# Optimization experiments

Hardware: AMD Instinct MI355X
Metric: run time of the kernel (lower is better)

Reference implementation:

```python
import jax, jax.numpy as jnp
import numpy as np

B, H, W, C = 2, 128, 128, 128
NS = 8                      # attn_num_splits
WH, WW = H // NS, W // NS   # window size 16x16
SH, SW = WH // 2, WW // 2   # shift sizes
HID = 2 * C * 4             # ffn hidden (in_channels = 2*d_model, expansion 4)
EPS = 1e-5


def _make_swin_mask():
    # Standard shifted-window attention mask: -100 between different regions.
    img = np.zeros((H, W), np.int32)
    cnt = 0
    for hs in (slice(0, -WH), slice(-WH, -SH), slice(-SH, None)):
        for ws in (slice(0, -WW), slice(-WW, -SW), slice(-SW, None)):
            img[hs, ws] = cnt
            cnt += 1
    ids = img.reshape(NS, WH, NS, WW).transpose(0, 2, 1, 3).reshape(NS * NS, WH * WW)
    mask = np.where(ids[:, None, :] != ids[:, :, None], -100.0, 0.0).astype(np.float32)
    return jnp.asarray(mask)  # (64, 256, 256)


def _layernorm(x, g, b):
    m = jnp.mean(x, axis=-1, keepdims=True)
    v = jnp.mean(jnp.square(x - m), axis=-1, keepdims=True)
    return (x - m) * jax.lax.rsqrt(v + EPS) * g + b


def setup_inputs() -> dict:
    key = jax.random.key(0)
    ks = jax.random.split(key, 8)
    s = 1.0 / np.sqrt(C)
    return {
        "source": jax.random.normal(ks[0], (B, H * W, C), jnp.float32),
        "target": jax.random.normal(ks[1], (B, H * W, C), jnp.float32),
        "Wq": jax.random.normal(ks[2], (C, C), jnp.float32) * s,
        "Wk": jax.random.normal(ks[3], (C, C), jnp.float32) * s,
        "Wv": jax.random.normal(ks[4], (C, C), jnp.float32) * s,
        "Wm": jax.random.normal(ks[5], (C, C), jnp.float32) * s,
        "g1": jnp.ones((C,), jnp.float32),
        "b1": jnp.zeros((C,), jnp.float32),
        "W1": jax.random.normal(ks[6], (2 * C, HID), jnp.float32) * (1.0 / np.sqrt(2 * C)),
        "W2": jax.random.normal(ks[7], (HID, C), jnp.float32) * (1.0 / np.sqrt(HID)),
        "g2": jnp.ones((C,), jnp.float32),
        "b2": jnp.zeros((C,), jnp.float32),
        "shifted_window_attn_mask": _make_swin_mask(),
        "height": H,
        "width": W,
        "attn_num_splits": NS,
    }


def reference(source, target, Wq, Wk, Wv, Wm, g1, b1, W1, W2, g2, b2,
              shifted_window_attn_mask, height, width, attn_num_splits):
    b, L, c = source.shape
    h, w, ns = height, width, attn_num_splits
    wh, ww = h // ns, w // ns
    sh, sw = wh // 2, ww // 2

    q = source @ Wq
    k = target @ Wk
    v = target @ Wv

    def to_windows(x):
        # (b, h*w, c) -> shifted -> (b, nWin, wh*ww, c)
        x = x.reshape(b, h, w, c)
        x = jnp.roll(x, (-sh, -sw), axis=(1, 2))
        x = x.reshape(b, ns, wh, ns, ww, c).transpose(0, 1, 3, 2, 4, 5)
        return x.reshape(b, ns * ns, wh * ww, c)

    qw, kw, vw = to_windows(q), to_windows(k), to_windows(v)
    scores = jnp.einsum('bnlc,bnmc->bnlm', qw, kw) / (c ** 0.5)
    scores = scores + shifted_window_attn_mask[None]  # broadcast over batch
    attn = jax.nn.softmax(scores, axis=-1)
    out = jnp.einsum('bnlm,bnmc->bnlc', attn, vw)

    # merge windows back and undo the shift
    out = out.reshape(b, ns, ns, wh, ww, c).transpose(0, 1, 3, 2, 4, 5).reshape(b, h, w, c)
    out = jnp.roll(out, (sh, sw), axis=(1, 2)).reshape(b, h * w, c)

    message = _layernorm(out @ Wm, g1, b1)
    ffn_in = jnp.concatenate([source, message], axis=-1)
    message = jax.nn.gelu(ffn_in @ W1, approximate=False) @ W2
    message = _layernorm(message, g2, b2)
    return source + message
```

## Files before the change

kernel.cpp:

```cpp
#include <hip/hip_runtime.h>
#include <math.h>
#include <stdint.h>


typedef unsigned short u16;
typedef __attribute__((ext_vector_type(8))) short bf16x8;
typedef __attribute__((ext_vector_type(4))) float f32x4;
typedef __attribute__((ext_vector_type(4))) short u16x4;
typedef __attribute__((ext_vector_type(2))) unsigned int u32x2;

__device__ __forceinline__ u16 f2b(float f) {
    unsigned int i = __float_as_uint(f);
    unsigned int r = (i + 0x7fffu + ((i >> 16) & 1u)) >> 16;
    return (u16)r;
}

__device__ __forceinline__ bf16x8 pk8(f32x4 a, f32x4 b) {
    union { bf16x8 v; unsigned u[4]; } r;
    asm("v_cvt_pk_bf16_f32 %0, %1, %2" : "=v"(r.u[0]) : "v"(a[0]), "v"(a[1]));
    asm("v_cvt_pk_bf16_f32 %0, %1, %2" : "=v"(r.u[1]) : "v"(a[2]), "v"(a[3]));
    asm("v_cvt_pk_bf16_f32 %0, %1, %2" : "=v"(r.u[2]) : "v"(b[0]), "v"(b[1]));
    asm("v_cvt_pk_bf16_f32 %0, %1, %2" : "=v"(r.u[3]) : "v"(b[2]), "v"(b[3]));
    return r.v;
}

__device__ __forceinline__ float gelu_e(float x) {
    float y = fabsf(x) * 0.70710678118f;
    float u = fmaf(y, fmaf(y, fmaf(y, fmaf(y, 0.078108f, 0.000972f),
                                   0.230389f), 0.278393f), 1.0f);
    u = u * u; u = u * u;
    float r = __builtin_amdgcn_rcpf(u);
    return fmaxf(x, 0.f) - 0.5f * fabsf(x) * r;
}

__device__ __forceinline__ void cp16(const void* g, void* l) {
    auto* gp = reinterpret_cast<const __attribute__((address_space(1))) unsigned int*>(
        reinterpret_cast<uintptr_t>(g));
    auto* lp = reinterpret_cast<__attribute__((address_space(3))) unsigned int*>(
        reinterpret_cast<uintptr_t>(l));
    __builtin_amdgcn_global_load_lds(gp, lp, 16, 0, 0);
}

__device__ __forceinline__ int win_map(int gm) {
    int b = gm >> 14, rr = gm & 16383;
    int win = rr >> 8, t = rr & 255;
    int wi = win >> 3, wj = win & 7, i = t >> 4, j = t & 15;
    int h = (wi * 16 + i + 8) & 127;
    int w = (wj * 16 + j + 8) & 127;
    return (b << 14) + h * 128 + w;
}

__global__ __launch_bounds__(256, 3)
void gemm_qkv(const float* __restrict__ srcf, const float* __restrict__ tgtf,
              const u16* __restrict__ Bt, u16* __restrict__ qw,
              u16* __restrict__ kw, u16* __restrict__ vwt)
{
    __shared__ __align__(16) u16 SMEM[17408];
    u16* Bs = SMEM;
    u16* Ts = SMEM;

    const int tid = threadIdx.x;
    const int w = tid >> 6, lane = tid & 63;
    const int lm = lane & 15, q = lane >> 4;
    const int wm = w >> 1, wn = w & 1;
    const int m0 = blockIdx.x * 128;
    const int y = blockIdx.y;
    const float* Af = (y == 0) ? srcf : tgtf;

#pragma unroll
    for (int s = 0; s < 4; ++s)
#pragma unroll
        for (int i = 0; i < 2; ++i) {
            int row = w * 32 + i * 16 + (lane >> 2);
            int kc = s * 32 + (lane & 3) * 8;
            cp16(Bt + (size_t)(y * 128 + row) * 128 + kc,
                 (void*)(Bs + (s * 128 + w * 32 + i * 16) * 32));
        }

    bf16x8 af[4][4];
#pragma unroll
    for (int t = 0; t < 4; ++t) {
        const float* ap = Af + (size_t)win_map(m0 + wm * 64 + t * 16 + lm) * 128;
#pragma unroll
        for (int s = 0; s < 4; ++s) {
            f32x4 a = *(const f32x4*)(ap + s * 32 + q * 8);
            f32x4 b = *(const f32x4*)(ap + s * 32 + q * 8 + 4);
            af[t][s] = pk8(a, b);
        }
    }
    __syncthreads();

    f32x4 acc[4][4] = {};
    __builtin_amdgcn_s_setprio(1);
#pragma unroll
    for (int s = 0; s < 4; ++s) {
        bf16x8 bfr[4];
#pragma unroll
        for (int t = 0; t < 4; ++t)
            bfr[t] = *(const bf16x8*)(Bs + (s * 128 + wn * 64 + t * 16 + lm) * 32 + q * 8);
#pragma unroll
        for (int mt = 0; mt < 4; ++mt)
#pragma unroll
            for (int nt = 0; nt < 4; ++nt)
                acc[mt][nt] = __builtin_amdgcn_mfma_f32_16x16x32_bf16(
                    af[mt][s], bfr[nt], acc[mt][nt], 0, 0, 0);
    }
    __builtin_amdgcn_s_setprio(0);

    __syncthreads();
#pragma unroll
    for (int mt = 0; mt < 4; ++mt)
#pragma unroll
        for (int nt = 0; nt < 4; ++nt)
#pragma unroll
            for (int r = 0; r < 4; ++r) {
                int rowl = wm * 64 + mt * 16 + q * 4 + r;
                int col = wn * 64 + nt * 16 + lm;
                int idx = (y == 2) ? col * 136 + rowl : rowl * 136 + col;
                Ts[idx] = f2b(acc[mt][nt][r]);
            }
    __syncthreads();
    const int c8 = (tid & 15) * 8;
#pragma unroll
    for (int i = 0; i < 8; ++i) {
        int rr = i * 16 + (tid >> 4);
        bf16x8 t = *(const bf16x8*)(Ts + rr * 136 + c8);
        if (y == 2) {
            int wix = m0 >> 8, tok0 = m0 & 255;
            *(bf16x8*)(vwt + (size_t)wix * 32768 + (size_t)rr * 256 + tok0 + c8) = t;
        } else {
            u16* Cv = (y == 0) ? qw : kw;
            *(bf16x8*)(Cv + (size_t)(m0 + rr) * 128 + c8) = t;
        }
    }
}

__global__ __launch_bounds__(256, 2)
void attn_msg(const u16* __restrict__ qw, const u16* __restrict__ kw,
              const u16* __restrict__ vt, const u16* __restrict__ wmt,
              const float* __restrict__ g, const float* __restrict__ bb,
              u16* __restrict__ msgb)
{
    __shared__ __align__(16) u16 Ps[64 * 264];
    __shared__ __align__(16) u16 B32[16384];

    const int tid = threadIdx.x, w = tid >> 6, lane = tid & 63;
    const int lm = lane & 15, q = lane >> 4;
    const int l4r = lane >> 2, l4c = (lane & 3) * 8;
    const int bid = blockIdx.x;
    const int qc = bid >> 7;
    const int gwin = bid & 127;
    const int win = gwin & 63, b = gwin >> 6;
    const int wi = win >> 3, wj = win & 7;
    const int q0 = qc * 64;
    const size_t wbase = (size_t)(b * 64 + win);
    const u16* kwb = kw + wbase * 256 * 128;
    const u16* qwb = qw + wbase * 256 * 128;
    const u16* vtb = vt + wbase * 128 * 256;

    u16* Qs = Ps;
#pragma unroll
    for (int i = 0; i < 4; ++i)
        cp16(qwb + (size_t)(q0 + w * 16 + l4r) * 128 + i * 32 + l4c,
             (void*)(Qs + (i * 64 + w * 16) * 32));
#pragma unroll
    for (int s = 0; s < 4; ++s)
#pragma unroll
        for (int i = 0; i < 2; ++i) {
            int tok = w * 32 + i * 16 + l4r;
            cp16(kwb + (size_t)tok * 128 + s * 32 + l4c,
                 (void*)(B32 + (s * 128 + w * 32 + i * 16) * 32));
        }
    __syncthreads();

    bf16x8 af[4];
#pragma unroll
    for (int kt = 0; kt < 4; ++kt)
        af[kt] = *(const bf16x8*)(Qs + (kt * 64 + w * 16 + lm) * 32 + q * 8);
    __syncthreads();

#pragma unroll
    for (int ss = 0; ss < 4; ++ss)
#pragma unroll
        for (int i = 0; i < 2; ++i) {
            int tok = 128 + w * 32 + i * 16 + l4r;
            cp16(kwb + (size_t)tok * 128 + ss * 32 + l4c,
                 (void*)(Ps + (ss * 128 + w * 32 + i * 16) * 32));
        }

    f32x4 s[16];
#pragma unroll
    for (int nt = 0; nt < 16; ++nt) { f32x4 z = {0.f, 0.f, 0.f, 0.f}; s[nt] = z; }
    __builtin_amdgcn_s_setprio(1);
#pragma unroll
    for (int kt = 0; kt < 4; ++kt)
#pragma unroll
        for (int nt = 0; nt < 8; ++nt) {
            bf16x8 bf = *(const bf16x8*)(B32 + (kt * 128 + nt * 16 + lm) * 32 + q * 8);
            s[nt] = __builtin_amdgcn_mfma_f32_16x16x32_bf16(af[kt], bf, s[nt], 0, 0, 0);
        }
    __builtin_amdgcn_s_setprio(0);
    __syncthreads();

#pragma unroll
    for (int tt = 0; tt < 4; ++tt)
#pragma unroll
        for (int i = 0; i < 2; ++i) {
            int ch = w * 32 + i * 16 + l4r;
            cp16(vtb + (size_t)ch * 256 + tt * 32 + l4c,
                 (void*)(B32 + (tt * 128 + w * 32 + i * 16) * 32));
        }
    __builtin_amdgcn_s_setprio(1);
#pragma unroll
    for (int kt = 0; kt < 4; ++kt)
#pragma unroll
        for (int nt = 8; nt < 16; ++nt) {
            bf16x8 bf = *(const bf16x8*)(Ps + (kt * 128 + (nt - 8) * 16 + lm) * 32 + q * 8);
            s[nt] = __builtin_amdgcn_mfma_f32_16x16x32_bf16(af[kt], bf, s[nt], 0, 0, 0);
        }
    __builtin_amdgcn_s_setprio(0);
    __syncthreads();

    int idk[16];
#pragma unroll
    for (int nt = 0; nt < 16; ++nt) {
        int rh = (wi == 7) ? ((nt >= 8) ? 2 : 1) : 0;
        int rw = (wj == 7) ? ((lm >= 8) ? 2 : 1) : 0;
        idk[nt] = rh * 3 + rw;
    }
    const float scale = 0.08838834764831845f;
#pragma unroll
    for (int r = 0; r < 4; ++r) {
        int tq = q0 + w * 16 + q * 4 + r;
        int iq = tq >> 4, jq = tq & 15;
        int rhq = (wi == 7) ? ((iq >= 8) ? 2 : 1) : 0;
        int rwq = (wj == 7) ? ((jq >= 8) ? 2 : 1) : 0;
        int idq = rhq * 3 + rwq;
        float sv[16];
        float mx = -1e30f;
#pragma unroll
        for (int nt = 0; nt < 16; ++nt) {
            float x = s[nt][r] * scale + ((idq != idk[nt]) ? -100.f : 0.f);
            sv[nt] = x; mx = fmaxf(mx, x);
        }
        mx = fmaxf(mx, __shfl_xor(mx, 1));
        mx = fmaxf(mx, __shfl_xor(mx, 2));
        mx = fmaxf(mx, __shfl_xor(mx, 4));
        mx = fmaxf(mx, __shfl_xor(mx, 8));
        float sum = 0.f;
#pragma unroll
        for (int nt = 0; nt < 16; ++nt) { float e = __expf(sv[nt] - mx); sv[nt] = e; sum += e; }
        sum += __shfl_xor(sum, 1);
        sum += __shfl_xor(sum, 2);
        sum += __shfl_xor(sum, 4);
        sum += __shfl_xor(sum, 8);
        float inv = 1.0f / sum;
#pragma unroll
        for (int nt = 0; nt < 16; ++nt)
            Ps[(w * 16 + q * 4 + r) * 264 + nt * 16 + lm] = f2b(sv[nt] * inv);
    }

    f32x4 o[8];
#pragma unroll
    for (int nt = 0; nt < 8; ++nt) { f32x4 z = {0.f, 0.f, 0.f, 0.f}; o[nt] = z; }
    __builtin_amdgcn_s_setprio(1);
#pragma unroll
    for (int tt = 0; tt < 4; ++tt) {
        bf16x8 pf = *(const bf16x8*)(Ps + (w * 16 + lm) * 264 + tt * 32 + q * 8);
#pragma unroll
        for (int nt = 0; nt < 8; ++nt) {
            bf16x8 vf = *(const bf16x8*)(B32 + (tt * 128 + nt * 16 + lm) * 32 + q * 8);
            o[nt] = __builtin_amdgcn_mfma_f32_16x16x32_bf16(pf, vf, o[nt], 0, 0, 0);
        }
    }
    __builtin_amdgcn_s_setprio(0);
    __syncthreads();
#pragma unroll
    for (int tt = 0; tt < 4; ++tt)
#pragma unroll
        for (int i = 0; i < 2; ++i) {
            int ch = w * 32 + i * 16 + l4r;
            cp16(vtb + (size_t)ch * 256 + 128 + tt * 32 + l4c,
                 (void*)(B32 + (tt * 128 + w * 32 + i * 16) * 32));
        }
    __syncthreads();
    __builtin_amdgcn_s_setprio(1);
#pragma unroll
    for (int tt = 4; tt < 8; ++tt) {
        bf16x8 pf = *(const bf16x8*)(Ps + (w * 16 + lm) * 264 + tt * 32 + q * 8);
#pragma unroll
        for (int nt = 0; nt < 8; ++nt) {
            bf16x8 vf = *(const bf16x8*)(B32 + ((tt - 4) * 128 + nt * 16 + lm) * 32 + q * 8);
            o[nt] = __builtin_amdgcn_mfma_f32_16x16x32_bf16(pf, vf, o[nt], 0, 0, 0);
        }
    }
    __builtin_amdgcn_s_setprio(0);
    __syncthreads();

#pragma unroll
    for (int ss = 0; ss < 4; ++ss)
#pragma unroll
        for (int i = 0; i < 2; ++i) {
            int n = w * 32 + i * 16 + l4r;
            cp16(wmt + (size_t)n * 128 + ss * 32 + l4c,
                 (void*)(B32 + (ss * 128 + w * 32 + i * 16) * 32));
        }
    u16* Ot = Ps;
#pragma unroll
    for (int r = 0; r < 4; ++r) {
        int rl = w * 16 + q * 4 + r;
#pragma unroll
        for (int nt = 0; nt < 8; ++nt)
            Ot[rl * 136 + nt * 16 + lm] = f2b(o[nt][r]);
    }
    __syncthreads();

    f32x4 macc[8];
#pragma unroll
    for (int n2 = 0; n2 < 8; ++n2) { f32x4 z = {0.f, 0.f, 0.f, 0.f}; macc[n2] = z; }
    __builtin_amdgcn_s_setprio(1);
#pragma unroll
    for (int kt = 0; kt < 4; ++kt) {
        bf16x8 paf = *(const bf16x8*)(Ot + (w * 16 + lm) * 136 + kt * 32 + q * 8);
#pragma unroll
        for (int n2 = 0; n2 < 8; ++n2) {
            bf16x8 wf = *(const bf16x8*)(B32 + (kt * 128 + n2 * 16 + lm) * 32 + q * 8);
            macc[n2] = __builtin_amdgcn_mfma_f32_16x16x32_bf16(paf, wf, macc[n2], 0, 0, 0);
        }
    }
    __builtin_amdgcn_s_setprio(0);

    float gv[8], bv[8];
#pragma unroll
    for (int n2 = 0; n2 < 8; ++n2) {
        int col = n2 * 16 + lm;
        gv[n2] = g[col]; bv[n2] = bb[col];
    }
#pragma unroll
    for (int r = 0; r < 4; ++r) {
        float s1 = 0.f, s2 = 0.f;
#pragma unroll
        for (int n2 = 0; n2 < 8; ++n2) {
            float v = macc[n2][r];
            s1 += v; s2 += v * v;
        }
        s1 += __shfl_xor(s1, 1); s2 += __shfl_xor(s2, 1);
        s1 += __shfl_xor(s1, 2); s2 += __shfl_xor(s2, 2);
        s1 += __shfl_xor(s1, 4); s2 += __shfl_xor(s2, 4);
        s1 += __shfl_xor(s1, 8); s2 += __shfl_xor(s2, 8);
        float mean = s1 * (1.f / 128.f);
        float var = fmaxf(s2 * (1.f / 128.f) - mean * mean, 0.f);
        float rs = rsqrtf(var + 1e-5f);
        int t = q0 + w * 16 + q * 4 + r;
        int ii = t >> 4, jj = t & 15;
        int h = (wi * 16 + ii + 8) & 127;
        int w2 = (wj * 16 + jj + 8) & 127;
        size_t orow = ((size_t)b * 16384 + h * 128 + w2) * 128;
#pragma unroll
        for (int n2 = 0; n2 < 8; ++n2)
            msgb[orow + n2 * 16 + lm] = f2b((macc[n2][r] - mean) * rs * gv[n2] + bv[n2]);
    }
}

__global__ __launch_bounds__(512, 4)
void fused_ffn(const float* __restrict__ A0f, const u16* __restrict__ A1,
               const u16* __restrict__ W1T, const u16* __restrict__ W2T,
               const float* __restrict__ g, const float* __restrict__ bb,
               const float* __restrict__ resid, float* __restrict__ outv)
{
    __shared__ __align__(16) u16 W1s[16384];
    __shared__ __align__(16) u16 W2s[16384];
    __shared__ __align__(16) u16 Gs[4096];

    const int tid = threadIdx.x;
    const int w = tid >> 6, lane = tid & 63;
    const int lm = lane & 15, q = lane >> 4;
    const int l4r = lane >> 2, l4c = (lane & 3) * 8;
    const int wm = w >> 2, wn = w & 3;
    const int m0 = blockIdx.x * 64;

    const u16* w1p = W1T + (size_t)l4r * 256 + w * 32 + l4c;
    const u16* w2p = W2T + (size_t)((w & 3) * 32 + l4r) * 1024 + (w >> 2) * 32 + l4c;
    u16* const w1d = W1s + (w * 64) * 32;
    u16* const w2d0 = W2s + (((w >> 2) * 128 + (w & 3) * 32)) * 32;
    u16* const w2d1 = w2d0 + 8192;

    bf16x8 areg[2][8];
#pragma unroll
    for (int mt = 0; mt < 2; ++mt) {
        const int row = m0 + wm * 32 + mt * 16 + lm;
        const float* ap = A0f + (size_t)row * 128;
#pragma unroll
        for (int ks = 0; ks < 4; ++ks) {
            f32x4 a = *(const f32x4*)(ap + ks * 32 + q * 8);
            f32x4 b = *(const f32x4*)(ap + ks * 32 + q * 8 + 4);
            areg[mt][ks] = pk8(a, b);
        }
#pragma unroll
        for (int ks = 4; ks < 8; ++ks)
            areg[mt][ks] = *(const bf16x8*)(
                A1 + (size_t)row * 128 + (ks & 3) * 32 + q * 8);
    }

#pragma unroll
    for (int i = 0; i < 4; ++i)
        cp16(w1p + (size_t)(i * 16) * 256, w1d + (i * 16) * 32);
#pragma unroll
    for (int i = 0; i < 2; ++i)
        cp16(w2p + (size_t)(i * 16) * 1024, w2d0 + (i * 16) * 32);
    w1p += 16384; w2p += 64;
    __syncthreads();

    f32x4 acc2[2][2] = {};
#pragma unroll 2
    for (int c = 0; c < 16; ++c) {
        const int cb = c & 1, nb = cb ^ 1;

        {
            f32x4 acc1[2] = {};
            __builtin_amdgcn_s_setprio(1);
#pragma unroll
            for (int ks = 0; ks < 8; ++ks) {
                bf16x8 w1f = *(const bf16x8*)(W1s + (ks * 64 + wn * 16 + lm) * 32 + q * 8);
#pragma unroll
                for (int mt = 0; mt < 2; ++mt)
                    acc1[mt] = __builtin_amdgcn_mfma_f32_16x16x32_bf16(
                        w1f, areg[mt][ks], acc1[mt], 0, 0, 0);
            }
            __builtin_amdgcn_s_setprio(0);
#pragma unroll
            for (int mt = 0; mt < 2; ++mt) {
                float g0 = gelu_e(acc1[mt][0]), g1 = gelu_e(acc1[mt][1]);
                float g2 = gelu_e(acc1[mt][2]), g3 = gelu_e(acc1[mt][3]);
                unsigned p0, p1;
                asm("v_cvt_pk_bf16_f32 %0, %1, %2" : "=v"(p0) : "v"(g0), "v"(g1));
                asm("v_cvt_pk_bf16_f32 %0, %1, %2" : "=v"(p1) : "v"(g2), "v"(g3));
                int tok = wm * 32 + mt * 16 + lm;
                int slot = (wn * 2 + (q >> 1)) ^ (tok & 7);
                u32x2 pk; pk[0] = p0; pk[1] = p1;
                *(u32x2*)(Gs + tok * 64 + slot * 8 + (q & 1) * 4) = pk;
            }
        }
        __syncthreads();

        if (c + 1 < 16) {
#pragma unroll
            for (int i = 0; i < 4; ++i)
                cp16(w1p + (size_t)(i * 16) * 256, w1d + (i * 16) * 32);
            u16* d = nb ? w2d1 : w2d0;
#pragma unroll
            for (int i = 0; i < 2; ++i)
                cp16(w2p + (size_t)(i * 16) * 1024, d + (i * 16) * 32);
        }
        w1p += 16384; w2p += 64;

        {
            const u16* W2c = W2s + cb * 8192;
            __builtin_amdgcn_s_setprio(1);
#pragma unroll
            for (int ks = 0; ks < 2; ++ks) {
                bf16x8 pa[2], wf[2];
#pragma unroll
                for (int mt = 0; mt < 2; ++mt) {
                    int tok = wm * 32 + mt * 16 + lm;
                    pa[mt] = *(const bf16x8*)(Gs + tok * 64 + (((ks * 4 + q) ^ (tok & 7)) * 8));
                }
#pragma unroll
                for (int nt = 0; nt < 2; ++nt)
                    wf[nt] = *(const bf16x8*)(W2c + (ks * 128 + wn * 32 + nt * 16 + lm) * 32 + q * 8);
#pragma unroll
                for (int mt = 0; mt < 2; ++mt)
#pragma unroll
                    for (int nt = 0; nt < 2; ++nt)
                        acc2[mt][nt] = __builtin_amdgcn_mfma_f32_16x16x32_bf16(
                            pa[mt], wf[nt], acc2[mt][nt], 0, 0, 0);
            }
            __builtin_amdgcn_s_setprio(0);
        }
        __syncthreads();
    }

    float* stats = (float*)Gs;
#pragma unroll
    for (int mt = 0; mt < 2; ++mt)
#pragma unroll
        for (int r = 0; r < 4; ++r) {
            float s1 = 0.f, s2 = 0.f;
#pragma unroll
            for (int nt = 0; nt < 2; ++nt) {
                float v = acc2[mt][nt][r];
                s1 += v; s2 += v * v;
            }
            s1 += __shfl_xor(s1, 1); s2 += __shfl_xor(s2, 1);
            s1 += __shfl_xor(s1, 2); s2 += __shfl_xor(s2, 2);
            s1 += __shfl_xor(s1, 4); s2 += __shfl_xor(s2, 4);
            s1 += __shfl_xor(s1, 8); s2 += __shfl_xor(s2, 8);
            if (lm == 0) {
                int row = wm * 32 + mt * 16 + q * 4 + r;
                stats[row * 8 + wn * 2] = s1;
                stats[row * 8 + wn * 2 + 1] = s2;
            }
        }
    __syncthreads();

    float gv[2], bv[2];
#pragma unroll
    for (int nt = 0; nt < 2; ++nt) {
        int col = wn * 32 + nt * 16 + lm;
        gv[nt] = g[col]; bv[nt] = bb[col];
    }
#pragma unroll
    for (int mt = 0; mt < 2; ++mt)
#pragma unroll
        for (int r = 0; r < 4; ++r) {
            int row = wm * 32 + mt * 16 + q * 4 + r;
            f32x4 st0 = *(const f32x4*)(stats + row * 8);
            f32x4 st1 = *(const f32x4*)(stats + row * 8 + 4);
            float s1 = st0[0] + st0[2] + st1[0] + st1[2];
            float s2 = st0[1] + st0[3] + st1[1] + st1[3];
            float mean = s1 * (1.f / 128.f);
            float var = fmaxf(s2 * (1.f / 128.f) - mean * mean, 0.f);
            float rs = rsqrtf(var + 1e-5f);
#pragma unroll
            for (int nt = 0; nt < 2; ++nt) {
                int col = wn * 32 + nt * 16 + lm;
                size_t gi = (size_t)(m0 + row) * 128 + col;
                outv[gi] = (acc2[mt][nt][r] - mean) * rs * gv[nt] + bv[nt] + resid[gi];
            }
        }
}

__global__ void prep_all(const float* __restrict__ Wq, const float* __restrict__ Wk,
                         const float* __restrict__ Wv, const float* __restrict__ Wm,
                         const float* __restrict__ W1, const float* __restrict__ W2,
                         u16* __restrict__ ws)
{
    __shared__ float T[64][65];
    int bx = blockIdx.x;
    const int t = threadIdx.x;
    const float* sp; u16* dst; int R, C, r0, c0;
    if (bx < 16) {
        int m = bx >> 2, tt = bx & 3;
        sp = (m == 0) ? Wq : (m == 1) ? Wk : (m == 2) ? Wv : Wm;
        R = 128; C = 128; r0 = (tt >> 1) * 64; c0 = (tt & 1) * 64;
        dst = ws + m * 16384;
    } else if (bx < 80) {
        int tt = bx - 16;
        sp = W1; R = 256; C = 1024;
        r0 = (tt >> 4) * 64; c0 = (tt & 15) * 64;
        dst = ws + 65536;
    } else {
        int tt = bx - 80;
        sp = W2; R = 1024; C = 128;
        r0 = (tt >> 1) * 64; c0 = (tt & 1) * 64;
        dst = ws + 327680;
    }
#pragma unroll
    for (int i = 0; i < 16; ++i) {
        int idx = i * 256 + t, r = idx >> 6, c = idx & 63;
        T[r][c] = sp[(size_t)(r0 + r) * C + c0 + c];
    }
    __syncthreads();
#pragma unroll
    for (int i = 0; i < 16; ++i) {
        int idx = i * 256 + t, n = idx >> 6, k = idx & 63;
        dst[(size_t)(c0 + n) * R + r0 + k] = f2b(T[k][n]);
    }
}

#define OFF_WQT  0u
#define OFF_WMT  49152u
#define OFF_W1T  65536u
#define OFF_W2T  327680u
#define OFF_QW   458752u
#define OFF_KW   4653056u
#define OFF_VWT  8847360u
#define OFF_MSGB 13041664u

extern "C" void kernel_launch(void* const* d_in, const int* in_sizes, int n_in,
                              void* d_out, int out_size, void* d_ws, size_t ws_size,
                              hipStream_t stream)
{
    (void)in_sizes; (void)n_in; (void)out_size; (void)ws_size;
    const float* source = (const float*)d_in[0];
    const float* target = (const float*)d_in[1];
    const float* Wq = (const float*)d_in[2];
    const float* Wk = (const float*)d_in[3];
    const float* Wv = (const float*)d_in[4];
    const float* Wm = (const float*)d_in[5];
    const float* g1 = (const float*)d_in[6];
    const float* b1 = (const float*)d_in[7];
    const float* W1 = (const float*)d_in[8];
    const float* W2 = (const float*)d_in[9];
    const float* g2 = (const float*)d_in[10];
    const float* b2 = (const float*)d_in[11];
    u16* ws = (u16*)d_ws;
    float* out = (float*)d_out;

    prep_all<<<112, 256, 0, stream>>>(Wq, Wk, Wv, Wm, W1, W2, ws);
    gemm_qkv<<<dim3(256, 3), 256, 0, stream>>>(
        source, target, ws + OFF_WQT,
        ws + OFF_QW, ws + OFF_KW, ws + OFF_VWT);
    attn_msg<<<512, 256, 0, stream>>>(
        ws + OFF_QW, ws + OFF_KW, ws + OFF_VWT, ws + OFF_WMT, g1, b1,
        ws + OFF_MSGB);
    fused_ffn<<<512, 512, 0, stream>>>(
        source, ws + OFF_MSGB, ws + OFF_W1T, ws + OFF_W2T,
        g2, b2, source, out);
}
```

Baseline: 187.3 us.

## Share target tile for K and V projections, pre-convert source to bf16

The QKV projection now runs with two grid rows instead of three. The block that loads the target tile computes both K and V from the same bf16 registers, so target is read and converted only once. The source activation is converted to bf16 once in the prep kernel and then reused by both the Q projection and the FFN, which halves their activation read bytes but adds an extra conversion pass and a workspace buffer. attn_msg also loads Q directly from global into registers and issues both K halves' async copies together, removing one shared-memory round trip and a barrier.

```diff
diff --git a/kernel.cpp b/kernel.cpp
--- a/kernel.cpp
+++ b/kernel.cpp
@@ -51,7 +51,7 @@
 }
 
 __global__ __launch_bounds__(256, 3)
-void gemm_qkv(const float* __restrict__ srcf, const float* __restrict__ tgtf,
+void gemm_qkv(const u16* __restrict__ srcb, const float* __restrict__ tgtf,
               const u16* __restrict__ Bt, u16* __restrict__ qw,
               u16* __restrict__ kw, u16* __restrict__ vwt)
 {
@@ -65,7 +65,7 @@
     const int wm = w >> 1, wn = w & 1;
     const int m0 = blockIdx.x * 128;
     const int y = blockIdx.y;
-    const float* Af = (y == 0) ? srcf : tgtf;
+    const int c8 = (tid & 15) * 8;
 
 #pragma unroll
     for (int s = 0; s < 4; ++s)
@@ -78,14 +78,24 @@
         }
 
     bf16x8 af[4][4];
-#pragma unroll
-    for (int t = 0; t < 4; ++t) {
-        const float* ap = Af + (size_t)win_map(m0 + wm * 64 + t * 16 + lm) * 128;
-#pragma unroll
-        for (int s = 0; s < 4; ++s) {
-            f32x4 a = *(const f32x4*)(ap + s * 32 + q * 8);
-            f32x4 b = *(const f32x4*)(ap + s * 32 + q * 8 + 4);
-            af[t][s] = pk8(a, b);
+    if (y == 0) {
+#pragma unroll
+        for (int t = 0; t < 4; ++t) {
+            const u16* ap = srcb + (size_t)win_map(m0 + wm * 64 + t * 16 + lm) * 128;
+#pragma unroll
+            for (int s = 0; s < 4; ++s)
+                af[t][s] = *(const bf16x8*)(ap + s * 32 + q * 8);
+        }
+    } else {
+#pragma unroll
+        for (int t = 0; t < 4; ++t) {
+            const float* ap = tgtf + (size_t)win_map(m0 + wm * 64 + t * 16 + lm) * 128;
+#pragma unroll
+            for (int s = 0; s < 4; ++s) {
+                f32x4 a = *(const f32x4*)(ap + s * 32 + q * 8);
+                f32x4 b = *(const f32x4*)(ap + s * 32 + q * 8 + 4);
+                af[t][s] = pk8(a, b);
+            }
         }
     }
     __syncthreads();
@@ -106,8 +116,8 @@
                     af[mt][s], bfr[nt], acc[mt][nt], 0, 0, 0);
     }
     __builtin_amdgcn_s_setprio(0);
-
-    __syncthreads();
+    __syncthreads();
+
 #pragma unroll
     for (int mt = 0; mt < 4; ++mt)
 #pragma unroll
@@ -116,21 +126,69 @@
             for (int r = 0; r < 4; ++r) {
                 int rowl = wm * 64 + mt * 16 + q * 4 + r;
                 int col = wn * 64 + nt * 16 + lm;
-                int idx = (y == 2) ? col * 136 + rowl : rowl * 136 + col;
-                Ts[idx] = f2b(acc[mt][nt][r]);
-            }
-    __syncthreads();
-    const int c8 = (tid & 15) * 8;
-#pragma unroll
-    for (int i = 0; i < 8; ++i) {
-        int rr = i * 16 + (tid >> 4);
-        bf16x8 t = *(const bf16x8*)(Ts + rr * 136 + c8);
-        if (y == 2) {
+                Ts[rowl * 136 + col] = f2b(acc[mt][nt][r]);
+            }
+    __syncthreads();
+    {
+        u16* Cv = (y == 0) ? qw : kw;
+#pragma unroll
+        for (int i = 0; i < 8; ++i) {
+            int rr = i * 16 + (tid >> 4);
+            bf16x8 t = *(const bf16x8*)(Ts + rr * 136 + c8);
+            *(bf16x8*)(Cv + (size_t)(m0 + rr) * 128 + c8) = t;
+        }
+    }
+
+    if (y == 1) {
+        __syncthreads();
+#pragma unroll
+        for (int s = 0; s < 4; ++s)
+#pragma unroll
+            for (int i = 0; i < 2; ++i) {
+                int row = w * 32 + i * 16 + (lane >> 2);
+                int kc = s * 32 + (lane & 3) * 8;
+                cp16(Bt + (size_t)(256 + row) * 128 + kc,
+                     (void*)(Bs + (s * 128 + w * 32 + i * 16) * 32));
+            }
+        __syncthreads();
+
+        f32x4 acc2[4][4] = {};
+        __builtin_amdgcn_s_setprio(1);
+#pragma unroll
+        for (int s = 0; s < 4; ++s) {
+            bf16x8 bfr[4];
+#pragma unroll
+            for (int t = 0; t < 4; ++t)
+                bfr[t] = *(const bf16x8*)(Bs + (s * 128 + wn * 64 + t * 16 + lm) * 32 + q * 8);
+#pragma unroll
+            for (int mt = 0; mt < 4; ++mt)
+#pragma unroll
+                for (int nt = 0; nt < 4; ++nt)
+                    acc2[mt][nt] = __builtin_amdgcn_mfma_f32_16x16x32_bf16(
+                        af[mt][s], bfr[nt], acc2[mt][nt], 0, 0, 0);
+        }
+        __builtin_amdgcn_s_setprio(0);
+        __syncthreads();
+
+#pragma unroll
+        for (int mt = 0; mt < 4; ++mt)
+#pragma unroll
+            for (int nt = 0; nt < 4; ++nt)
+#pragma unroll
+                for (int r = 0; r < 4; ++r) {
+                    int rowl = wm * 64 + mt * 16 + q * 4 + r;
+                    int col = wn * 64 + nt * 16 + lm;
+                    Ts[col * 136 + rowl] = f2b(acc2[mt][nt][r]);
+                }
+        __syncthreads();
+        {
             int wix = m0 >> 8, tok0 = m0 & 255;
-            *(bf16x8*)(vwt + (size_t)wix * 32768 + (size_t)rr * 256 + tok0 + c8) = t;
-        } else {
-            u16* Cv = (y == 0) ? qw : kw;
-            *(bf16x8*)(Cv + (size_t)(m0 + rr) * 128 + c8) = t;
+#pragma unroll
+            for (int i = 0; i < 8; ++i) {
+                int rr = i * 16 + (tid >> 4);
+                bf16x8 t = *(const bf16x8*)(Ts + rr * 136 + c8);
+                *(bf16x8*)(vwt + (size_t)wix * 32768 + (size_t)rr * 256 + tok0 + c8) = t;
+            }
         }
     }
 }
@@ -158,11 +216,6 @@
     const u16* qwb = qw + wbase * 256 * 128;
     const u16* vtb = vt + wbase * 128 * 256;
 
-    u16* Qs = Ps;
-#pragma unroll
-    for (int i = 0; i < 4; ++i)
-        cp16(qwb + (size_t)(q0 + w * 16 + l4r) * 128 + i * 32 + l4c,
-             (void*)(Qs + (i * 64 + w * 16) * 32));
 #pragma unroll
     for (int s = 0; s < 4; ++s)
 #pragma unroll
@@ -170,23 +223,15 @@
             int tok = w * 32 + i * 16 + l4r;
             cp16(kwb + (size_t)tok * 128 + s * 32 + l4c,
                  (void*)(B32 + (s * 128 + w * 32 + i * 16) * 32));
-        }
-    __syncthreads();
+            cp16(kwb + (size_t)(128 + tok) * 128 + s * 32 + l4c,
+                 (void*)(Ps + (s * 128 + w * 32 + i * 16) * 32));
+        }
 
     bf16x8 af[4];
 #pragma unroll
     for (int kt = 0; kt < 4; ++kt)
-        af[kt] = *(const bf16x8*)(Qs + (kt * 64 + w * 16 + lm) * 32 + q * 8);
-    __syncthreads();
-
-#pragma unroll
-    for (int ss = 0; ss < 4; ++ss)
-#pragma unroll
-        for (int i = 0; i < 2; ++i) {
-            int tok = 128 + w * 32 + i * 16 + l4r;
-            cp16(kwb + (size_t)tok * 128 + ss * 32 + l4c,
-                 (void*)(Ps + (ss * 128 + w * 32 + i * 16) * 32));
-        }
+        af[kt] = *(const bf16x8*)(qwb + (size_t)(q0 + w * 16 + lm) * 128 + kt * 32 + q * 8);
+    __syncthreads();
 
     f32x4 s[16];
 #pragma unroll
@@ -363,7 +408,7 @@
 }
 
 __global__ __launch_bounds__(512, 4)
-void fused_ffn(const float* __restrict__ A0f, const u16* __restrict__ A1,
+void fused_ffn(const u16* __restrict__ A0, const u16* __restrict__ A1,
                const u16* __restrict__ W1T, const u16* __restrict__ W2T,
                const float* __restrict__ g, const float* __restrict__ bb,
                const float* __restrict__ resid, float* __restrict__ outv)
@@ -387,20 +432,13 @@
 
     bf16x8 areg[2][8];
 #pragma unroll
-    for (int mt = 0; mt < 2; ++mt) {
-        const int row = m0 + wm * 32 + mt * 16 + lm;
-        const float* ap = A0f + (size_t)row * 128;
-#pragma unroll
-        for (int ks = 0; ks < 4; ++ks) {
-            f32x4 a = *(const f32x4*)(ap + ks * 32 + q * 8);
-            f32x4 b = *(const f32x4*)(ap + ks * 32 + q * 8 + 4);
-            areg[mt][ks] = pk8(a, b);
-        }
-#pragma unroll
-        for (int ks = 4; ks < 8; ++ks)
+    for (int mt = 0; mt < 2; ++mt)
+#pragma unroll
+        for (int ks = 0; ks < 8; ++ks) {
+            const u16* Ab = (ks < 4) ? A0 : A1;
             areg[mt][ks] = *(const bf16x8*)(
-                A1 + (size_t)row * 128 + (ks & 3) * 32 + q * 8);
-    }
+                Ab + (size_t)(m0 + wm * 32 + mt * 16 + lm) * 128 + (ks & 3) * 32 + q * 8);
+        }
 
 #pragma unroll
     for (int i = 0; i < 4; ++i)
@@ -533,38 +571,47 @@
 __global__ void prep_all(const float* __restrict__ Wq, const float* __restrict__ Wk,
                          const float* __restrict__ Wv, const float* __restrict__ Wm,
                          const float* __restrict__ W1, const float* __restrict__ W2,
-                         u16* __restrict__ ws)
+                         const float* __restrict__ src, u16* __restrict__ ws,
+                         u16* __restrict__ srcb)
 {
-    __shared__ float T[64][65];
     int bx = blockIdx.x;
-    const int t = threadIdx.x;
-    const float* sp; u16* dst; int R, C, r0, c0;
-    if (bx < 16) {
-        int m = bx >> 2, tt = bx & 3;
-        sp = (m == 0) ? Wq : (m == 1) ? Wk : (m == 2) ? Wv : Wm;
-        R = 128; C = 128; r0 = (tt >> 1) * 64; c0 = (tt & 1) * 64;
-        dst = ws + m * 16384;
-    } else if (bx < 80) {
-        int tt = bx - 16;
-        sp = W1; R = 256; C = 1024;
-        r0 = (tt >> 4) * 64; c0 = (tt & 15) * 64;
-        dst = ws + 65536;
+    if (bx < 112) {
+        __shared__ float T[64][65];
+        const int t = threadIdx.x;
+        const float* sp; u16* dst; int R, C, r0, c0;
+        if (bx < 16) {
+            int m = bx >> 2, tt = bx & 3;
+            sp = (m == 0) ? Wq : (m == 1) ? Wk : (m == 2) ? Wv : Wm;
+            R = 128; C = 128; r0 = (tt >> 1) * 64; c0 = (tt & 1) * 64;
+            dst = ws + m * 16384;
+        } else if (bx < 80) {
+            int tt = bx - 16;
+            sp = W1; R = 256; C = 1024;
+            r0 = (tt >> 4) * 64; c0 = (tt & 15) * 64;
+            dst = ws + 65536;
+        } else {
+            int tt = bx - 80;
+            sp = W2; R = 1024; C = 128;
+            r0 = (tt >> 1) * 64; c0 = (tt & 1) * 64;
+            dst = ws + 327680;
+        }
+#pragma unroll
+        for (int i = 0; i < 16; ++i) {
+            int idx = i * 256 + t, r = idx >> 6, c = idx & 63;
+            T[r][c] = sp[(size_t)(r0 + r) * C + c0 + c];
+        }
+        __syncthreads();
+#pragma unroll
+        for (int i = 0; i < 16; ++i) {
+            int idx = i * 256 + t, n = idx >> 6, k = idx & 63;
+            dst[(size_t)(c0 + n) * R + r0 + k] = f2b(T[k][n]);
+        }
     } else {
-        int tt = bx - 80;
-        sp = W2; R = 1024; C = 128;
-        r0 = (tt >> 1) * 64; c0 = (tt & 1) * 64;
-        dst = ws + 327680;
-    }
-#pragma unroll
-    for (int i = 0; i < 16; ++i) {
-        int idx = i * 256 + t, r = idx >> 6, c = idx & 63;
-        T[r][c] = sp[(size_t)(r0 + r) * C + c0 + c];
-    }
-    __syncthreads();
-#pragma unroll
-    for (int i = 0; i < 16; ++i) {
-        int idx = i * 256 + t, n = idx >> 6, k = idx & 63;
-        dst[(size_t)(c0 + n) * R + r0 + k] = f2b(T[k][n]);
+        int idx = (bx - 112) * 256 + threadIdx.x;
+        int i = idx * 4;
+        f32x4 v = *(const f32x4*)(src + i);
+        u16x4 o; o[0] = f2b(v[0]); o[1] = f2b(v[1]); o[2] = f2b(v[2]); o[3] = f2b(v[3]);
+        *(u16x4*)(srcb + i) = o;
     }
 }
 
@@ -572,10 +619,11 @@
 #define OFF_WMT  49152u
 #define OFF_W1T  65536u
 #define OFF_W2T  327680u
-#define OFF_QW   458752u
-#define OFF_KW   4653056u
-#define OFF_VWT  8847360u
-#define OFF_MSGB 13041664u
+#define OFF_SRCB 458752u
+#define OFF_QW   4653056u
+#define OFF_KW   8847360u
+#define OFF_VWT  13041664u
+#define OFF_MSGB 17235968u
 
 extern "C" void kernel_launch(void* const* d_in, const int* in_sizes, int n_in,
                               void* d_out, int out_size, void* d_ws, size_t ws_size,
@@ -597,14 +645,15 @@
     u16* ws = (u16*)d_ws;
     float* out = (float*)d_out;
 
-    prep_all<<<112, 256, 0, stream>>>(Wq, Wk, Wv, Wm, W1, W2, ws);
-    gemm_qkv<<<dim3(256, 3), 256, 0, stream>>>(
-        source, target, ws + OFF_WQT,
+    prep_all<<<4208, 256, 0, stream>>>(Wq, Wk, Wv, Wm, W1, W2, source,
+                                       ws, ws + OFF_SRCB);
+    gemm_qkv<<<dim3(256, 2), 256, 0, stream>>>(
+        ws + OFF_SRCB, target, ws + OFF_WQT,
         ws + OFF_QW, ws + OFF_KW, ws + OFF_VWT);
     attn_msg<<<512, 256, 0, stream>>>(
         ws + OFF_QW, ws + OFF_KW, ws + OFF_VWT, ws + OFF_WMT, g1, b1,
         ws + OFF_MSGB);
     fused_ffn<<<512, 512, 0, stream>>>(
-        source, ws + OFF_MSGB, ws + OFF_W1T, ws + OFF_W2T,
+        ws + OFF_SRCB, ws + OFF_MSGB, ws + OFF_W1T, ws + OFF_W2T,
         g2, b2, source, out);
 }
```

Result: no change. 187.0 us (median of 3 runs) (-0.2%).
